# Performance work log

Measured on AMD Instinct MI355X. Metric: run time of the kernel, lower is better.

The kernel has to match this reference:

```python
import jax, jax.numpy as jnp
import numpy as np

K_NEIGHBOURS = 40  # includes self; self is dropped after top-k


def setup_inputs() -> dict:
    key = jax.random.key(0)
    ks = jax.random.split(key, 4)
    B, V, F_in = 4, 4096, 64
    P, S, F_out = 64, 4, 64
    x = jax.random.normal(ks[0], (B, V, F_in), dtype=jnp.float32)
    Wf = jax.random.normal(ks[1], (F_in, P), dtype=jnp.float32) / np.sqrt(F_in)
    bf = jnp.zeros((P,), dtype=jnp.float32)
    Ws = jax.random.normal(ks[2], (F_in, S), dtype=jnp.float32) / np.sqrt(F_in)
    bs = jnp.zeros((S,), dtype=jnp.float32)
    Wo = jax.random.normal(ks[3], (F_in + 2 * P, F_out), dtype=jnp.float32) / np.sqrt(F_in + 2 * P)
    bo = jnpp = jnp.zeros((F_out,), dtype=jnp.float32)
    return {"x": x, "Wf": Wf, "bf": bf, "Ws": Ws, "bs": bs, "Wo": Wo, "bo": bo}


def _euclidean_squared(c):
    # c: [B, V, S] -> [B, V, V] squared pairwise distances
    sq = jnp.sum(c * c, axis=-1)  # [B, V]
    d2 = sq[:, :, None] + sq[:, None, :] - 2.0 * jnp.einsum('bvs,bus->bvu', c, c)
    return d2


def reference(x, Wf, bf, Ws, bs, Wo, bo):
    # learned spatial coordinates and propagated features
    coords = x @ Ws + bs            # [B, V, S]
    feats = x @ Wf + bf             # [B, V, P]

    d2 = _euclidean_squared(coords)                 # [B, V, V]
    neg_vals, idx = jax.lax.top_k(-d2, K_NEIGHBOURS)  # closest first (self at 0)
    nbr_idx = idx[:, :, 1:]                         # [B, V, K-1]
    dist = -neg_vals[:, :, 1:]                      # [B, V, K-1] (>= 0)

    # gauss_of_lin(d * 10) = exp(-|10 d|)
    w = jnp.exp(-jnp.abs(dist * 10.0))              # [B, V, K-1]

    # gather neighbour features per batch: [B, V, K-1, P]
    nf = jax.vmap(lambda f, i: f[i])(feats, nbr_idx)
    nf = nf * w[..., None]

    collected = jnp.concatenate([jnp.max(nf, axis=2), jnp.mean(nf, axis=2)], axis=-1)  # [B, V, 2P]
    updated = jnp.concatenate([x, collected], axis=-1)  # [B, V, F_in + 2P]
    return jnp.tanh(updated @ Wo + bo)
```

## Files before the change

kernel.cpp:

```cpp
#include <hip/hip_runtime.h>
#include <cmath>

#define BB  4
#define VV  4096
#define KK  40
#define FIN 64

typedef float v2f __attribute__((ext_vector_type(2)));

__global__ __launch_bounds__(256, 8) void prep_kernel(
    const float* __restrict__ x, const float* __restrict__ Wf,
    const float* __restrict__ bf, const float* __restrict__ Ws,
    const float* __restrict__ bs,
    float* __restrict__ coords, float* __restrict__ sq,
    float* __restrict__ feats)
{
    int lane = threadIdx.x & 63;
    int wid  = threadIdx.x >> 6;
    int row0 = (blockIdx.x * 4 + wid) * 2;
    const float* xr = x + (size_t)row0 * FIN;

    float rx0 = xr[lane];
    float rx1 = xr[64 + lane];

    float a0 = 0.f, a1 = 0.f;
    #pragma unroll
    for (int k = 0; k < FIN; ++k) {
        float wf = Wf[k * 64 + lane];
        a0 = fmaf(__uint_as_float(
             __builtin_amdgcn_readlane(__float_as_uint(rx0), k)), wf, a0);
        a1 = fmaf(__uint_as_float(
             __builtin_amdgcn_readlane(__float_as_uint(rx1), k)), wf, a1);
    }
    float bfl = bf[lane];
    feats[(size_t)(row0 + 0) * 64 + lane] = a0 + bfl;
    feats[(size_t)(row0 + 1) * 64 + lane] = a1 + bfl;

    int r  = lane >> 5;
    int s  = (lane >> 3) & 3;
    int kc = lane & 7;
    const float* xrr = x + (size_t)(row0 + r) * FIN + kc * 8;
    const float* wsr = Ws + kc * 8 * 4 + s;
    float c = 0.f;
    #pragma unroll
    for (int k = 0; k < 8; ++k)
        c = fmaf(xrr[k], wsr[k * 4], c);
    c += __shfl_xor(c, 1, 64);
    c += __shfl_xor(c, 2, 64);
    c += __shfl_xor(c, 4, 64);
    float val = c + bs[s];
    if ((lane & 7) == 0) coords[(size_t)(row0 + r) * 4 + s] = val;
    float p = val * val;
    p += __shfl_xor(p, 8, 64);
    p += __shfl_xor(p, 16, 64);
    if ((lane & 31) == 0) sq[row0 + r] = p;
}

__device__ __forceinline__ unsigned umed3(unsigned a, unsigned b, unsigned c)
{
    unsigned d;
    asm("v_med3_u32 %0, %1, %2, %3" : "=v"(d) : "v"(a), "v"(b), "v"(c));
    return d;
}

__device__ __forceinline__ unsigned bfi_key(unsigned maskv, unsigned d2b,
                                            unsigned u)
{
    unsigned d;
    asm("v_bfi_b32 %0, %1, %2, %3" : "=v"(d) : "v"(maskv), "v"(d2b), "v"(u));
    return d;
}

__device__ __forceinline__ int cnt_lt4(unsigned m0, unsigned m1,
                                       unsigned m2, unsigned m3,
                                       unsigned cand)
{
    return (int)__popcll(__ballot(m0 < cand))
         + (int)__popcll(__ballot(m1 < cand))
         + (int)__popcll(__ballot(m2 < cand))
         + (int)__popcll(__ballot(m3 < cand));
}

__device__ __forceinline__ void select_thresh4(
    unsigned m00, unsigned m01, unsigned m02, unsigned m03,
    unsigned m10, unsigned m11, unsigned m12, unsigned m13,
    unsigned m20, unsigned m21, unsigned m22, unsigned m23,
    unsigned m30, unsigned m31, unsigned m32, unsigned m33,
    unsigned& Ms0, unsigned& Ms1, unsigned& Ms2, unsigned& Ms3)
{
    unsigned M0 = 0u, M1 = 0u, M2 = 0u, M3 = 0u;
    #pragma unroll
    for (int bit = 30; bit >= 12; --bit) {
        unsigned b = 1u << bit;
        unsigned c0 = M0 | b, c1 = M1 | b, c2 = M2 | b, c3 = M3 | b;
        int n0 = cnt_lt4(m00, m01, m02, m03, c0);
        int n1 = cnt_lt4(m10, m11, m12, m13, c1);
        int n2 = cnt_lt4(m20, m21, m22, m23, c2);
        int n3 = cnt_lt4(m30, m31, m32, m33, c3);
        if (n0 <= 39) M0 = c0;
        if (n1 <= 39) M1 = c1;
        if (n2 <= 39) M2 = c2;
        if (n3 <= 39) M3 = c3;
    }
    Ms0 = M0 | 0xFFFu; Ms1 = M1 | 0xFFFu;
    Ms2 = M2 | 0xFFFu; Ms3 = M3 | 0xFFFu;
    if (cnt_lt4(m00, m01, m02, m03, M0 + 4096u) != 40) {
        #pragma unroll
        for (int bit = 11; bit >= 0; --bit) {
            unsigned cand = M0 | (1u << bit);
            if (cnt_lt4(m00, m01, m02, m03, cand) <= 39) M0 = cand;
        }
        Ms0 = M0;
    }
    if (cnt_lt4(m10, m11, m12, m13, M1 + 4096u) != 40) {
        #pragma unroll
        for (int bit = 11; bit >= 0; --bit) {
            unsigned cand = M1 | (1u << bit);
            if (cnt_lt4(m10, m11, m12, m13, cand) <= 39) M1 = cand;
        }
        Ms1 = M1;
    }
    if (cnt_lt4(m20, m21, m22, m23, M2 + 4096u) != 40) {
        #pragma unroll
        for (int bit = 11; bit >= 0; --bit) {
            unsigned cand = M2 | (1u << bit);
            if (cnt_lt4(m20, m21, m22, m23, cand) <= 39) M2 = cand;
        }
        Ms2 = M2;
    }
    if (cnt_lt4(m30, m31, m32, m33, M3 + 4096u) != 40) {
        #pragma unroll
        for (int bit = 11; bit >= 0; --bit) {
            unsigned cand = M3 | (1u << bit);
            if (cnt_lt4(m30, m31, m32, m33, cand) <= 39) M3 = cand;
        }
        Ms3 = M3;
    }
}

__device__ __forceinline__ void compact4(unsigned m0, unsigned m1,
                                         unsigned m2, unsigned m3,
                                         unsigned Msel, unsigned mn,
                                         uint2* dst)
{
    int base = 0;
    unsigned kk = m0;
    #pragma unroll
    for (int i = 0; i < 4; ++i) {
        bool pred = (kk <= Msel) && (kk != mn);
        unsigned long long mask = __ballot(pred);
        unsigned pos = (unsigned)base +
            __builtin_amdgcn_mbcnt_hi((unsigned)(mask >> 32),
                __builtin_amdgcn_mbcnt_lo((unsigned)mask, 0u));
        if (pred) {
            float d2a = __uint_as_float(kk & 0xFFFFF000u);
            float w   = __expf(-10.f * d2a);
            dst[pos] = make_uint2((kk & 4095u) << 8, __float_as_uint(w));
        }
        base += (int)__popcll(mask);
        kk = (i == 0) ? m1 : (i == 1) ? m2 : m3;
    }
}

__global__ __launch_bounds__(256, 4) void gravnet_kernel(
    const float* __restrict__ x, const float* __restrict__ coords,
    const float* __restrict__ sq, const float* __restrict__ feats,
    const float* __restrict__ Wo, const float* __restrict__ bo,
    float* __restrict__ out)
{
    int lane = threadIdx.x & 63;
    int w    = threadIdx.x >> 6;
    int bid  = (int)((blockIdx.x & 7) * 128 + (blockIdx.x >> 3));
    int gw   = bid * 4 + w;
    int qb   = gw * 4;
    int b    = qb >> 12;
    int v0   = qb & (VV - 1);

    __shared__ __align__(16) char smem[12288];
    uint2* s_nb  = (uint2*)(smem + w * 3072);
    float* s_upd = (float*)(smem + w * 3072);

    const float4* cb  = (const float4*)(coords + (size_t)b * VV * 4);
    const float*  sqb = sq + (size_t)b * VV;

    float4 cq0 = cb[v0],     cq1 = cb[v0 + 1];
    float4 cq2 = cb[v0 + 2], cq3 = cb[v0 + 3];
    v2f nxA = (v2f){-2.f * cq0.x, -2.f * cq1.x};
    v2f nyA = (v2f){-2.f * cq0.y, -2.f * cq1.y};
    v2f nzA = (v2f){-2.f * cq0.z, -2.f * cq1.z};
    v2f nwA = (v2f){-2.f * cq0.w, -2.f * cq1.w};
    v2f hsA = (v2f){sqb[v0], sqb[v0 + 1]};
    v2f nxB = (v2f){-2.f * cq2.x, -2.f * cq3.x};
    v2f nyB = (v2f){-2.f * cq2.y, -2.f * cq3.y};
    v2f nzB = (v2f){-2.f * cq2.z, -2.f * cq3.z};
    v2f nwB = (v2f){-2.f * cq2.w, -2.f * cq3.w};
    v2f hsB = (v2f){sqb[v0 + 2], sqb[v0 + 3]};

    unsigned k00 = ~0u, k01 = ~0u, k02 = ~0u, k03 = ~0u;
    unsigned k10 = ~0u, k11 = ~0u, k12 = ~0u, k13 = ~0u;
    unsigned k20 = ~0u, k21 = ~0u, k22 = ~0u, k23 = ~0u;
    unsigned k30 = ~0u, k31 = ~0u, k32 = ~0u, k33 = ~0u;

    unsigned maskv = 0xFFFFF000u;

    #pragma unroll 4
    for (int i = 0; i < 64; ++i) {
        int u = i * 64 + lane;
        float4 cu = cb[u];
        float squ = sqb[u];
        v2f accA = hsA + (v2f){squ, squ};
        accA = __builtin_elementwise_fma(nxA, (v2f){cu.x, cu.x}, accA);
        accA = __builtin_elementwise_fma(nyA, (v2f){cu.y, cu.y}, accA);
        accA = __builtin_elementwise_fma(nzA, (v2f){cu.z, cu.z}, accA);
        accA = __builtin_elementwise_fma(nwA, (v2f){cu.w, cu.w}, accA);
        v2f accB = hsB + (v2f){squ, squ};
        accB = __builtin_elementwise_fma(nxB, (v2f){cu.x, cu.x}, accB);
        accB = __builtin_elementwise_fma(nyB, (v2f){cu.y, cu.y}, accB);
        accB = __builtin_elementwise_fma(nzB, (v2f){cu.z, cu.z}, accB);
        accB = __builtin_elementwise_fma(nwB, (v2f){cu.w, cu.w}, accB);

        {
            float d2 = fmaxf(accA.x, 0.f);
            unsigned k = bfi_key(maskv, __float_as_uint(d2), (unsigned)u);
            unsigned n1 = umed3(k00, k01, k);
            unsigned n2 = umed3(k01, k02, k);
            unsigned n3 = umed3(k02, k03, k);
            k00 = min(k00, k); k01 = n1; k02 = n2; k03 = n3;
        }
        {
            float d2 = fmaxf(accA.y, 0.f);
            unsigned k = bfi_key(maskv, __float_as_uint(d2), (unsigned)u);
            unsigned n1 = umed3(k10, k11, k);
            unsigned n2 = umed3(k11, k12, k);
            unsigned n3 = umed3(k12, k13, k);
            k10 = min(k10, k); k11 = n1; k12 = n2; k13 = n3;
        }
        {
            float d2 = fmaxf(accB.x, 0.f);
            unsigned k = bfi_key(maskv, __float_as_uint(d2), (unsigned)u);
            unsigned n1 = umed3(k20, k21, k);
            unsigned n2 = umed3(k21, k22, k);
            unsigned n3 = umed3(k22, k23, k);
            k20 = min(k20, k); k21 = n1; k22 = n2; k23 = n3;
        }
        {
            float d2 = fmaxf(accB.y, 0.f);
            unsigned k = bfi_key(maskv, __float_as_uint(d2), (unsigned)u);
            unsigned n1 = umed3(k30, k31, k);
            unsigned n2 = umed3(k31, k32, k);
            unsigned n3 = umed3(k32, k33, k);
            k30 = min(k30, k); k31 = n1; k32 = n2; k33 = n3;
        }
    }

    unsigned mn0 = k00, mn1 = k10, mn2 = k20, mn3 = k30;
    #pragma unroll
    for (int off = 32; off >= 1; off >>= 1) {
        unsigned o0 = __shfl_xor(mn0, off, 64);
        unsigned o1 = __shfl_xor(mn1, off, 64);
        unsigned o2 = __shfl_xor(mn2, off, 64);
        unsigned o3 = __shfl_xor(mn3, off, 64);
        mn0 = min(mn0, o0); mn1 = min(mn1, o1);
        mn2 = min(mn2, o2); mn3 = min(mn3, o3);
    }

    unsigned Ms0, Ms1, Ms2, Ms3;
    select_thresh4(k00, k01, k02, k03, k10, k11, k12, k13,
                   k20, k21, k22, k23, k30, k31, k32, k33,
                   Ms0, Ms1, Ms2, Ms3);
    compact4(k00, k01, k02, k03, Ms0, mn0, &s_nb[0 * KK]);
    compact4(k10, k11, k12, k13, Ms1, mn1, &s_nb[1 * KK]);
    compact4(k20, k21, k22, k23, Ms2, mn2, &s_nb[2 * KK]);
    compact4(k30, k31, k32, k33, Ms3, mn3, &s_nb[3 * KK]);

    const float* fb  = feats + (size_t)b * VV * 64;
    unsigned lane4 = (unsigned)lane << 2;
    const uint4* nb0 = (const uint4*)&s_nb[0 * KK];
    const uint4* nb1 = (const uint4*)&s_nb[1 * KK];
    const uint4* nb2 = (const uint4*)&s_nb[2 * KK];
    const uint4* nb3 = (const uint4*)&s_nb[3 * KK];
    v2f vmax01 = (v2f){-INFINITY, -INFINITY};
    v2f vsum01 = (v2f){0.f, 0.f};
    v2f vmax23 = (v2f){-INFINITY, -INFINITY};
    v2f vsum23 = (v2f){0.f, 0.f};
    #pragma unroll 4
    for (int jp = 0; jp < 19; ++jp) {
        uint4 a = nb0[jp];
        uint4 c = nb1[jp];
        uint4 e = nb2[jp];
        uint4 g = nb3[jp];
        float f0a = *(const float*)((const char*)fb + (a.x + lane4));
        float f1a = *(const float*)((const char*)fb + (c.x + lane4));
        float f2a = *(const float*)((const char*)fb + (e.x + lane4));
        float f3a = *(const float*)((const char*)fb + (g.x + lane4));
        float f0b = *(const float*)((const char*)fb + (a.z + lane4));
        float f1b = *(const float*)((const char*)fb + (c.z + lane4));
        float f2b = *(const float*)((const char*)fb + (e.z + lane4));
        float f3b = *(const float*)((const char*)fb + (g.z + lane4));
        v2f ga01 = (v2f){f0a, f1a} *
                   (v2f){__uint_as_float(a.y), __uint_as_float(c.y)};
        v2f gb01 = (v2f){f0b, f1b} *
                   (v2f){__uint_as_float(a.w), __uint_as_float(c.w)};
        v2f ga23 = (v2f){f2a, f3a} *
                   (v2f){__uint_as_float(e.y), __uint_as_float(g.y)};
        v2f gb23 = (v2f){f2b, f3b} *
                   (v2f){__uint_as_float(e.w), __uint_as_float(g.w)};
        vmax01 = __builtin_elementwise_max(vmax01,
                 __builtin_elementwise_max(ga01, gb01));
        vsum01 += ga01 + gb01;
        vmax23 = __builtin_elementwise_max(vmax23,
                 __builtin_elementwise_max(ga23, gb23));
        vsum23 += ga23 + gb23;
    }
    {
        uint2 n0 = s_nb[0 * KK + 38];
        uint2 n1 = s_nb[1 * KK + 38];
        uint2 n2 = s_nb[2 * KK + 38];
        uint2 n3 = s_nb[3 * KK + 38];
        float f0 = *(const float*)((const char*)fb + (n0.x + lane4));
        float f1 = *(const float*)((const char*)fb + (n1.x + lane4));
        float f2 = *(const float*)((const char*)fb + (n2.x + lane4));
        float f3 = *(const float*)((const char*)fb + (n3.x + lane4));
        v2f g01 = (v2f){f0, f1} *
                  (v2f){__uint_as_float(n0.y), __uint_as_float(n1.y)};
        v2f g23 = (v2f){f2, f3} *
                  (v2f){__uint_as_float(n2.y), __uint_as_float(n3.y)};
        vmax01 = __builtin_elementwise_max(vmax01, g01);
        vsum01 += g01;
        vmax23 = __builtin_elementwise_max(vmax23, g23);
        vsum23 += g23;
    }

    int q0g = qb, q1g = qb + 1, q2g = qb + 2, q3g = qb + 3;
    float* sb = s_upd;
    *(float4*)&sb[lane * 4] =
        make_float4(x[(size_t)q0g * 64 + lane], x[(size_t)q1g * 64 + lane],
                    x[(size_t)q2g * 64 + lane], x[(size_t)q3g * 64 + lane]);
    *(float4*)&sb[256 + lane * 4] =
        make_float4(vmax01.x, vmax01.y, vmax23.x, vmax23.y);
    *(float4*)&sb[512 + lane * 4] =
        make_float4(vsum01.x * (1.0f / 39.0f), vsum01.y * (1.0f / 39.0f),
                    vsum23.x * (1.0f / 39.0f), vsum23.y * (1.0f / 39.0f));

    float bol = bo[lane];
    v2f acc01 = (v2f){bol, bol};
    v2f acc23 = (v2f){bol, bol};
    #pragma unroll 8
    for (int j = 0; j < 192; ++j) {
        float wo = Wo[j * 64 + lane];
        float4 up = *(const float4*)&sb[j * 4];
        acc01 = __builtin_elementwise_fma((v2f){up.x, up.y},
                                          (v2f){wo, wo}, acc01);
        acc23 = __builtin_elementwise_fma((v2f){up.z, up.w},
                                          (v2f){wo, wo}, acc23);
    }
    float e0t = __expf(2.f * acc01.x);
    float e1t = __expf(2.f * acc01.y);
    float e2t = __expf(2.f * acc23.x);
    float e3t = __expf(2.f * acc23.y);
    out[(size_t)q0g * 64 + lane] = 1.f - __fdividef(2.f, e0t + 1.f);
    out[(size_t)q1g * 64 + lane] = 1.f - __fdividef(2.f, e1t + 1.f);
    out[(size_t)q2g * 64 + lane] = 1.f - __fdividef(2.f, e2t + 1.f);
    out[(size_t)q3g * 64 + lane] = 1.f - __fdividef(2.f, e3t + 1.f);
}

extern "C" void kernel_launch(void* const* d_in, const int* in_sizes, int n_in,
                              void* d_out, int out_size, void* d_ws, size_t ws_size,
                              hipStream_t stream)
{
    (void)in_sizes; (void)n_in; (void)out_size; (void)ws_size;
    const float* x  = (const float*)d_in[0];
    const float* Wf = (const float*)d_in[1];
    const float* bf = (const float*)d_in[2];
    const float* Ws = (const float*)d_in[3];
    const float* bs = (const float*)d_in[4];
    const float* Wo = (const float*)d_in[5];
    const float* bo = (const float*)d_in[6];
    float* out = (float*)d_out;

    float* coords = (float*)d_ws;
    float* sq     = coords + (size_t)BB * VV * 4;
    float* feats  = sq + (size_t)BB * VV;

    prep_kernel<<<BB * VV / 8, 256, 0, stream>>>(x, Wf, bf, Ws, bs,
                                                 coords, sq, feats);
    gravnet_kernel<<<BB * VV / 16, 256, 0, stream>>>(x, coords, sq, feats,
                                                     Wo, bo, out);
}
```

Measured before the change: 119.1 us.

## Stage candidate coordinates through double-buffered LDS tiles shared across the block

The distance scan now cooperatively loads 256-point tiles of coordinates and squared norms into shared memory, double-buffered, with the next tile's global load issued before computing on the current one. All four waves read from LDS instead of each wave separately loading every candidate from global/L2. This adds a block-wide barrier per tile and LDS traffic, and reuses the same shared region that later holds the neighbour lists.

```diff
diff --git a/kernel.cpp b/kernel.cpp
--- a/kernel.cpp
+++ b/kernel.cpp
@@ -168,8 +168,9 @@
     const float* __restrict__ Wo, const float* __restrict__ bo,
     float* __restrict__ out)
 {
-    int lane = threadIdx.x & 63;
-    int w    = threadIdx.x >> 6;
+    int tid  = threadIdx.x;
+    int lane = tid & 63;
+    int w    = tid >> 6;
     int bid  = (int)((blockIdx.x & 7) * 128 + (blockIdx.x >> 3));
     int gw   = bid * 4 + w;
     int qb   = gw * 4;
@@ -177,6 +178,8 @@
     int v0   = qb & (VV - 1);
 
     __shared__ __align__(16) char smem[12288];
+    float4* s_c4 = (float4*)smem;
+    float*  s_sq = (float*)(smem + 8192);
     uint2* s_nb  = (uint2*)(smem + w * 3072);
     float* s_upd = (float*)(smem + w * 3072);
 
@@ -203,54 +206,79 @@
 
     unsigned maskv = 0xFFFFF000u;
 
-    #pragma unroll 4
-    for (int i = 0; i < 64; ++i) {
-        int u = i * 64 + lane;
-        float4 cu = cb[u];
-        float squ = sqb[u];
-        v2f accA = hsA + (v2f){squ, squ};
-        accA = __builtin_elementwise_fma(nxA, (v2f){cu.x, cu.x}, accA);
-        accA = __builtin_elementwise_fma(nyA, (v2f){cu.y, cu.y}, accA);
-        accA = __builtin_elementwise_fma(nzA, (v2f){cu.z, cu.z}, accA);
-        accA = __builtin_elementwise_fma(nwA, (v2f){cu.w, cu.w}, accA);
-        v2f accB = hsB + (v2f){squ, squ};
-        accB = __builtin_elementwise_fma(nxB, (v2f){cu.x, cu.x}, accB);
-        accB = __builtin_elementwise_fma(nyB, (v2f){cu.y, cu.y}, accB);
-        accB = __builtin_elementwise_fma(nzB, (v2f){cu.z, cu.z}, accB);
-        accB = __builtin_elementwise_fma(nwB, (v2f){cu.w, cu.w}, accB);
-
-        {
-            float d2 = fmaxf(accA.x, 0.f);
-            unsigned k = bfi_key(maskv, __float_as_uint(d2), (unsigned)u);
-            unsigned n1 = umed3(k00, k01, k);
-            unsigned n2 = umed3(k01, k02, k);
-            unsigned n3 = umed3(k02, k03, k);
-            k00 = min(k00, k); k01 = n1; k02 = n2; k03 = n3;
-        }
-        {
-            float d2 = fmaxf(accA.y, 0.f);
-            unsigned k = bfi_key(maskv, __float_as_uint(d2), (unsigned)u);
-            unsigned n1 = umed3(k10, k11, k);
-            unsigned n2 = umed3(k11, k12, k);
-            unsigned n3 = umed3(k12, k13, k);
-            k10 = min(k10, k); k11 = n1; k12 = n2; k13 = n3;
-        }
-        {
-            float d2 = fmaxf(accB.x, 0.f);
-            unsigned k = bfi_key(maskv, __float_as_uint(d2), (unsigned)u);
-            unsigned n1 = umed3(k20, k21, k);
-            unsigned n2 = umed3(k21, k22, k);
-            unsigned n3 = umed3(k22, k23, k);
-            k20 = min(k20, k); k21 = n1; k22 = n2; k23 = n3;
-        }
-        {
-            float d2 = fmaxf(accB.y, 0.f);
-            unsigned k = bfi_key(maskv, __float_as_uint(d2), (unsigned)u);
-            unsigned n1 = umed3(k30, k31, k);
-            unsigned n2 = umed3(k31, k32, k);
-            unsigned n3 = umed3(k32, k33, k);
-            k30 = min(k30, k); k31 = n1; k32 = n2; k33 = n3;
-        }
+    {
+        float4 pv4 = cb[tid];
+        float  psq = sqb[tid];
+        s_c4[tid] = pv4;
+        s_sq[tid] = psq;
+    }
+    __syncthreads();
+
+    #pragma unroll 1
+    for (int t = 0; t < 16; ++t) {
+        int cur = t & 1;
+        float4 nv4; float nsq;
+        if (t < 15) {
+            nv4 = cb[(t + 1) * 256 + tid];
+            nsq = sqb[(t + 1) * 256 + tid];
+        }
+        const float4* c4t = s_c4 + cur * 256;
+        const float*  sqt = s_sq + cur * 256;
+        #pragma unroll
+        for (int it = 0; it < 4; ++it) {
+            int idx = it * 64 + lane;
+            float4 cu = c4t[idx];
+            float squ = sqt[idx];
+            unsigned u = (unsigned)(t * 256 + idx);
+            v2f accA = hsA + (v2f){squ, squ};
+            accA = __builtin_elementwise_fma(nxA, (v2f){cu.x, cu.x}, accA);
+            accA = __builtin_elementwise_fma(nyA, (v2f){cu.y, cu.y}, accA);
+            accA = __builtin_elementwise_fma(nzA, (v2f){cu.z, cu.z}, accA);
+            accA = __builtin_elementwise_fma(nwA, (v2f){cu.w, cu.w}, accA);
+            v2f accB = hsB + (v2f){squ, squ};
+            accB = __builtin_elementwise_fma(nxB, (v2f){cu.x, cu.x}, accB);
+            accB = __builtin_elementwise_fma(nyB, (v2f){cu.y, cu.y}, accB);
+            accB = __builtin_elementwise_fma(nzB, (v2f){cu.z, cu.z}, accB);
+            accB = __builtin_elementwise_fma(nwB, (v2f){cu.w, cu.w}, accB);
+
+            {
+                float d2 = fmaxf(accA.x, 0.f);
+                unsigned k = bfi_key(maskv, __float_as_uint(d2), u);
+                unsigned n1 = umed3(k00, k01, k);
+                unsigned n2 = umed3(k01, k02, k);
+                unsigned n3 = umed3(k02, k03, k);
+                k00 = min(k00, k); k01 = n1; k02 = n2; k03 = n3;
+            }
+            {
+                float d2 = fmaxf(accA.y, 0.f);
+                unsigned k = bfi_key(maskv, __float_as_uint(d2), u);
+                unsigned n1 = umed3(k10, k11, k);
+                unsigned n2 = umed3(k11, k12, k);
+                unsigned n3 = umed3(k12, k13, k);
+                k10 = min(k10, k); k11 = n1; k12 = n2; k13 = n3;
+            }
+            {
+                float d2 = fmaxf(accB.x, 0.f);
+                unsigned k = bfi_key(maskv, __float_as_uint(d2), u);
+                unsigned n1 = umed3(k20, k21, k);
+                unsigned n2 = umed3(k21, k22, k);
+                unsigned n3 = umed3(k22, k23, k);
+                k20 = min(k20, k); k21 = n1; k22 = n2; k23 = n3;
+            }
+            {
+                float d2 = fmaxf(accB.y, 0.f);
+                unsigned k = bfi_key(maskv, __float_as_uint(d2), u);
+                unsigned n1 = umed3(k30, k31, k);
+                unsigned n2 = umed3(k31, k32, k);
+                unsigned n3 = umed3(k32, k33, k);
+                k30 = min(k30, k); k31 = n1; k32 = n2; k33 = n3;
+            }
+        }
+        if (t < 15) {
+            s_c4[(cur ^ 1) * 256 + tid] = nv4;
+            s_sq[(cur ^ 1) * 256 + tid] = nsq;
+        }
+        __syncthreads();
     }
 
     unsigned mn0 = k00, mn1 = k10, mn2 = k20, mn3 = k30;
```

After: 121.4 us. About the same (+1.9%).

## Fuse prep projection into main kernel with per-batch atomic grid barrier

Applied to the files above, without the earlier changes.

Merges the projection kernel into the kNN/aggregation kernel. Each block first computes features, coordinates and squared norms for its own 16 rows, then waits on a per-batch atomic counter until all 256 blocks of that batch have finished. This removes one kernel launch and the gap between the two kernels, at the cost of a memset and a spin-wait barrier. The barrier assumes all 1024 blocks can be resident at once, since launch bounds allow 4 blocks per CU; otherwise it could deadlock.

```diff
diff --git a/kernel.cpp b/kernel.cpp
--- a/kernel.cpp
+++ b/kernel.cpp
@@ -7,54 +7,6 @@
 #define FIN 64
 
 typedef float v2f __attribute__((ext_vector_type(2)));
-
-__global__ __launch_bounds__(256, 8) void prep_kernel(
-    const float* __restrict__ x, const float* __restrict__ Wf,
-    const float* __restrict__ bf, const float* __restrict__ Ws,
-    const float* __restrict__ bs,
-    float* __restrict__ coords, float* __restrict__ sq,
-    float* __restrict__ feats)
-{
-    int lane = threadIdx.x & 63;
-    int wid  = threadIdx.x >> 6;
-    int row0 = (blockIdx.x * 4 + wid) * 2;
-    const float* xr = x + (size_t)row0 * FIN;
-
-    float rx0 = xr[lane];
-    float rx1 = xr[64 + lane];
-
-    float a0 = 0.f, a1 = 0.f;
-    #pragma unroll
-    for (int k = 0; k < FIN; ++k) {
-        float wf = Wf[k * 64 + lane];
-        a0 = fmaf(__uint_as_float(
-             __builtin_amdgcn_readlane(__float_as_uint(rx0), k)), wf, a0);
-        a1 = fmaf(__uint_as_float(
-             __builtin_amdgcn_readlane(__float_as_uint(rx1), k)), wf, a1);
-    }
-    float bfl = bf[lane];
-    feats[(size_t)(row0 + 0) * 64 + lane] = a0 + bfl;
-    feats[(size_t)(row0 + 1) * 64 + lane] = a1 + bfl;
-
-    int r  = lane >> 5;
-    int s  = (lane >> 3) & 3;
-    int kc = lane & 7;
-    const float* xrr = x + (size_t)(row0 + r) * FIN + kc * 8;
-    const float* wsr = Ws + kc * 8 * 4 + s;
-    float c = 0.f;
-    #pragma unroll
-    for (int k = 0; k < 8; ++k)
-        c = fmaf(xrr[k], wsr[k * 4], c);
-    c += __shfl_xor(c, 1, 64);
-    c += __shfl_xor(c, 2, 64);
-    c += __shfl_xor(c, 4, 64);
-    float val = c + bs[s];
-    if ((lane & 7) == 0) coords[(size_t)(row0 + r) * 4 + s] = val;
-    float p = val * val;
-    p += __shfl_xor(p, 8, 64);
-    p += __shfl_xor(p, 16, 64);
-    if ((lane & 31) == 0) sq[row0 + r] = p;
-}
 
 __device__ __forceinline__ unsigned umed3(unsigned a, unsigned b, unsigned c)
 {
@@ -91,8 +43,8 @@
     unsigned M0 = 0u, M1 = 0u, M2 = 0u, M3 = 0u;
     #pragma unroll
     for (int bit = 30; bit >= 12; --bit) {
-        unsigned b = 1u << bit;
-        unsigned c0 = M0 | b, c1 = M1 | b, c2 = M2 | b, c3 = M3 | b;
+        unsigned bm = 1u << bit;
+        unsigned c0 = M0 | bm, c1 = M1 | bm, c2 = M2 | bm, c3 = M3 | bm;
         int n0 = cnt_lt4(m00, m01, m02, m03, c0);
         int n1 = cnt_lt4(m10, m11, m12, m13, c1);
         int n2 = cnt_lt4(m20, m21, m22, m23, c2);
@@ -162,23 +114,85 @@
     }
 }
 
-__global__ __launch_bounds__(256, 4) void gravnet_kernel(
-    const float* __restrict__ x, const float* __restrict__ coords,
-    const float* __restrict__ sq, const float* __restrict__ feats,
+__global__ __launch_bounds__(256, 4) void fused_kernel(
+    const float* __restrict__ x, const float* __restrict__ Wf,
+    const float* __restrict__ bf, const float* __restrict__ Ws,
+    const float* __restrict__ bs,
     const float* __restrict__ Wo, const float* __restrict__ bo,
+    float* __restrict__ coords, float* __restrict__ sq,
+    float* __restrict__ feats, unsigned* __restrict__ cnt,
     float* __restrict__ out)
 {
-    int lane = threadIdx.x & 63;
-    int w    = threadIdx.x >> 6;
+    int tid  = threadIdx.x;
+    int lane = tid & 63;
+    int w    = tid >> 6;
     int bid  = (int)((blockIdx.x & 7) * 128 + (blockIdx.x >> 3));
-    int gw   = bid * 4 + w;
-    int qb   = gw * 4;
+    int qb   = bid * 16 + w * 4;
     int b    = qb >> 12;
     int v0   = qb & (VV - 1);
 
     __shared__ __align__(16) char smem[12288];
     uint2* s_nb  = (uint2*)(smem + w * 3072);
     float* s_upd = (float*)(smem + w * 3072);
+
+    {
+        int row0 = qb;
+        const float* xr = x + (size_t)row0 * FIN;
+        float rx0 = xr[lane];
+        float rx1 = xr[64  + lane];
+        float rx2 = xr[128 + lane];
+        float rx3 = xr[192 + lane];
+
+        float a0 = 0.f, a1 = 0.f, a2 = 0.f, a3 = 0.f;
+        #pragma unroll
+        for (int k = 0; k < FIN; ++k) {
+            float wf = Wf[k * 64 + lane];
+            a0 = fmaf(__uint_as_float(
+                 __builtin_amdgcn_readlane(__float_as_uint(rx0), k)), wf, a0);
+            a1 = fmaf(__uint_as_float(
+                 __builtin_amdgcn_readlane(__float_as_uint(rx1), k)), wf, a1);
+            a2 = fmaf(__uint_as_float(
+                 __builtin_amdgcn_readlane(__float_as_uint(rx2), k)), wf, a2);
+            a3 = fmaf(__uint_as_float(
+                 __builtin_amdgcn_readlane(__float_as_uint(rx3), k)), wf, a3);
+        }
+        float bfl = bf[lane];
+        feats[(size_t)(row0 + 0) * 64 + lane] = a0 + bfl;
+        feats[(size_t)(row0 + 1) * 64 + lane] = a1 + bfl;
+        feats[(size_t)(row0 + 2) * 64 + lane] = a2 + bfl;
+        feats[(size_t)(row0 + 3) * 64 + lane] = a3 + bfl;
+
+        int r  = lane >> 4;
+        int s  = (lane >> 2) & 3;
+        int kc = lane & 3;
+        const float* xrr = x + (size_t)(row0 + r) * FIN + kc * 16;
+        const float* wsr = Ws + kc * 16 * 4 + s;
+        float c = 0.f;
+        #pragma unroll
+        for (int k = 0; k < 16; ++k)
+            c = fmaf(xrr[k], wsr[k * 4], c);
+        c += __shfl_xor(c, 1, 64);
+        c += __shfl_xor(c, 2, 64);
+        float val = c + bs[s];
+        if ((lane & 3) == 0) coords[(size_t)(row0 + r) * 4 + s] = val;
+        float p = val * val;
+        p += __shfl_xor(p, 4, 64);
+        p += __shfl_xor(p, 8, 64);
+        if ((lane & 15) == 0) sq[row0 + r] = p;
+    }
+
+    __threadfence();
+    __syncthreads();
+    if (tid == 0) {
+        __hip_atomic_fetch_add(&cnt[b], 1u, __ATOMIC_RELEASE,
+                               __HIP_MEMORY_SCOPE_AGENT);
+        while (__hip_atomic_load(&cnt[b], __ATOMIC_ACQUIRE,
+                                 __HIP_MEMORY_SCOPE_AGENT) < 256u)
+            __builtin_amdgcn_s_sleep(8);
+    }
+    __syncthreads();
+    (void)__hip_atomic_load(&cnt[b], __ATOMIC_ACQUIRE,
+                            __HIP_MEMORY_SCOPE_AGENT);
 
     const float4* cb  = (const float4*)(coords + (size_t)b * VV * 4);
     const float*  sqb = sq + (size_t)b * VV;
@@ -381,9 +395,9 @@
     float* coords = (float*)d_ws;
     float* sq     = coords + (size_t)BB * VV * 4;
     float* feats  = sq + (size_t)BB * VV;
-
-    prep_kernel<<<BB * VV / 8, 256, 0, stream>>>(x, Wf, bf, Ws, bs,
-                                                 coords, sq, feats);
-    gravnet_kernel<<<BB * VV / 16, 256, 0, stream>>>(x, coords, sq, feats,
-                                                     Wo, bo, out);
-}
+    unsigned* cnt = (unsigned*)(feats + (size_t)BB * VV * 64);
+
+    hipMemsetAsync(cnt, 0, BB * sizeof(unsigned), stream);
+    fused_kernel<<<BB * VV / 16, 256, 0, stream>>>(
+        x, Wf, bf, Ws, bs, Wo, bo, coords, sq, feats, cnt, out);
+}
```

Result: slower. 311.7 us (+161.7%).
